# Kernel optimization log

Hardware: AMD Instinct MI355X
Metric: run time of the kernel (lower is better)

## Reference

```python
import jax, jax.numpy as jnp
import numpy as np

K = 256
HEADS = 4

def setup_inputs() -> dict:
    key = jax.random.key(0)
    ks = jax.random.split(key, 6)
    x = jax.random.normal(ks[0], (4, 4096, K), dtype=jnp.float32)
    scale = 1.0 / np.sqrt(K)
    Wq = jax.random.normal(ks[1], (K, K), dtype=jnp.float32) * scale
    Wk = jax.random.normal(ks[2], (K, K), dtype=jnp.float32) * scale
    Wv = jax.random.normal(ks[3], (K, K), dtype=jnp.float32) * scale
    Wu = jax.random.normal(ks[4], (K, K), dtype=jnp.float32) * scale
    bu = jax.random.normal(ks[5], (K,), dtype=jnp.float32) * scale
    return {"x": x, "Wq": Wq, "Wk": Wk, "Wv": Wv, "Wu": Wu, "bu": bu}

def reference(x, Wq, Wk, Wv, Wu, bu):
    b, t, e = x.shape
    h = HEADS
    s = e // h
    # torch Linear: y = x @ W.T
    q = (x @ Wq.T).reshape(b, t, h, s)
    k = (x @ Wk.T).reshape(b, t, h, s)
    v = (x @ Wv.T).reshape(b, t, h, s)
    # scores: [b, h, t, t]
    dot = jnp.einsum('bihs,bjhs->bhij', q, k) / jnp.sqrt(jnp.float32(s))
    # NOTE: original code calls masked_fill (non in-place) and discards the
    # result, so the causal mask has NO effect. Faithful: no mask.
    attn = jax.nn.softmax(dot, axis=-1)
    out = jnp.einsum('bhij,bjhs->bihs', attn, v).reshape(b, t, e)
    return out @ Wu.T + bu
```

## Files before the change

### kernel.cpp

```cpp
#include <hip/hip_runtime.h>

typedef unsigned short u16;
typedef __attribute__((ext_vector_type(8))) __bf16 bf16x8;
typedef __attribute__((ext_vector_type(4))) float f32x4;
typedef __attribute__((ext_vector_type(4))) unsigned int u32x4;
typedef __attribute__((ext_vector_type(2))) unsigned int u32x2;

#define GLD16(g, l) __builtin_amdgcn_global_load_lds( \
    (const __attribute__((address_space(1))) unsigned int*)(g), \
    (__attribute__((address_space(3))) unsigned int*)(l), 16, 0, 0)

__device__ __forceinline__ u16 f2bf(float f) {
    unsigned u = __builtin_bit_cast(unsigned, f);
    unsigned r = u + 0x7fffu + ((u >> 16) & 1u);
    return (u16)(r >> 16);
}

__global__ __launch_bounds__(256) void cvt_bf16(const float* __restrict__ src,
                                                u16* __restrict__ dst, int n8) {
    int i = blockIdx.x * 256 + threadIdx.x;
    if (i >= n8) return;
    const float4* s = (const float4*)src;
    float4 a = s[2 * i], b = s[2 * i + 1];
    union { u16 u[8]; u32x4 v; } o;
    o.u[0] = f2bf(a.x); o.u[1] = f2bf(a.y); o.u[2] = f2bf(a.z); o.u[3] = f2bf(a.w);
    o.u[4] = f2bf(b.x); o.u[5] = f2bf(b.y); o.u[6] = f2bf(b.z); o.u[7] = f2bf(b.w);
    ((u32x4*)dst)[i] = o.v;
}

__global__ __launch_bounds__(256) void cvt_w4(const float* __restrict__ Wq,
                                              const float* __restrict__ Wk,
                                              const float* __restrict__ Wv,
                                              const float* __restrict__ Wu,
                                              u16* __restrict__ dst, float qscale) {
    int i = blockIdx.x * 256 + threadIdx.x;
    int widx = i >> 13, j = i & 8191;
    const float* src = (widx == 0) ? Wq : (widx == 1) ? Wk : (widx == 2) ? Wv : Wu;
    float scale = (widx == 0) ? qscale : 1.0f;
    const float4* s = (const float4*)src;
    float4 a = s[2 * j], b = s[2 * j + 1];
    union { u16 u[8]; u32x4 v; } o;
    o.u[0] = f2bf(a.x * scale); o.u[1] = f2bf(a.y * scale);
    o.u[2] = f2bf(a.z * scale); o.u[3] = f2bf(a.w * scale);
    o.u[4] = f2bf(b.x * scale); o.u[5] = f2bf(b.y * scale);
    o.u[6] = f2bf(b.z * scale); o.u[7] = f2bf(b.w * scale);
    ((u32x4*)dst)[i] = o.v;
}

template <int F32OUT>
__device__ __forceinline__ void gemm_core(const u16* __restrict__ A,
                                          const u16* __restrict__ B,
                                          void* __restrict__ Cout,
                                          const float* __restrict__ bias,
                                          size_t ldc, u16* As, u16* Bs) {
    const int tid = threadIdx.x;
    const int w = tid >> 6, l = tid & 63;
    const int lo = l & 15, hi = l >> 4;
    const size_t m0 = (size_t)blockIdx.x * 128;
    const int n0 = blockIdx.y * 128;
    const int wm = (w >> 1) * 64, wn = (w & 1) * 64;

    f32x4 acc[4][4] = {};

    {
#pragma unroll
        for (int i = 0; i < 2; ++i) {
            int cidx = (w * 2 + i) * 64 + l;
            int row = cidx >> 2, c = cidx & 3;
            GLD16(A + (m0 + row) * 256 + c * 8, &As[(w * 2 + i) * 512]);
            GLD16(B + (size_t)(n0 + row) * 256 + c * 8, &Bs[(w * 2 + i) * 512]);
        }
    }
    int buf = 0;
#pragma unroll 1
    for (int k0 = 0; k0 < 8; ++k0) {
        __syncthreads();
        if (k0 < 7) {
#pragma unroll
            for (int i = 0; i < 2; ++i) {
                int cidx = (w * 2 + i) * 64 + l;
                int row = cidx >> 2, c = cidx & 3;
                GLD16(A + (m0 + row) * 256 + (k0 + 1) * 32 + c * 8, &As[(buf ^ 1) * 4096 + (w * 2 + i) * 512]);
                GLD16(B + (size_t)(n0 + row) * 256 + (k0 + 1) * 32 + c * 8, &Bs[(buf ^ 1) * 4096 + (w * 2 + i) * 512]);
            }
        }
        bf16x8 af[4], bg[4];
#pragma unroll
        for (int mt = 0; mt < 4; ++mt)
            af[mt] = *(const bf16x8*)&As[buf * 4096 + (wm + mt * 16 + lo) * 32 + hi * 8];
#pragma unroll
        for (int nt = 0; nt < 4; ++nt)
            bg[nt] = *(const bf16x8*)&Bs[buf * 4096 + (wn + nt * 16 + lo) * 32 + hi * 8];
        __builtin_amdgcn_s_setprio(1);
#pragma unroll
        for (int mt = 0; mt < 4; ++mt)
#pragma unroll
            for (int nt = 0; nt < 4; ++nt)
                acc[mt][nt] = __builtin_amdgcn_mfma_f32_16x16x32_bf16(af[mt], bg[nt], acc[mt][nt], 0, 0, 0);
        __builtin_amdgcn_s_setprio(0);
        buf ^= 1;
    }

    const int r0 = hi * 4;
#pragma unroll
    for (int mt = 0; mt < 4; ++mt) {
#pragma unroll
        for (int nt = 0; nt < 4; ++nt) {
            int col = n0 + wn + nt * 16 + lo;
#pragma unroll
            for (int r = 0; r < 4; ++r) {
                size_t row = m0 + wm + mt * 16 + r0 + r;
                if (F32OUT) {
                    ((float*)Cout)[row * ldc + col] = acc[mt][nt][r] + bias[col];
                } else {
                    ((u16*)Cout)[row * ldc + col] = f2bf(acc[mt][nt][r]);
                }
            }
        }
    }
}

__global__ __launch_bounds__(256) void gemm_qk(const u16* __restrict__ xb,
                                               const u16* __restrict__ wqb,
                                               const u16* __restrict__ wkb,
                                               u16* __restrict__ qb,
                                               u16* __restrict__ kb) {
    __shared__ u16 As[2 * 4096];
    __shared__ u16 Bs[2 * 4096];
    if (blockIdx.z == 0)
        gemm_core<0>(xb, wqb, qb, nullptr, 256, As, Bs);
    else
        gemm_core<0>(xb, wkb, kb, nullptr, 256, As, Bs);
}

template <int F32OUT>
__global__ __launch_bounds__(256) void gemm_one(const u16* __restrict__ A,
                                                const u16* __restrict__ B,
                                                void* __restrict__ C,
                                                const float* __restrict__ bias,
                                                size_t ldc) {
    __shared__ u16 As[2 * 4096];
    __shared__ u16 Bs[2 * 4096];
    gemm_core<F32OUT>(A, B, C, bias, ldc, As, Bs);
}

__global__ __launch_bounds__(256, 2) void attn_fwd(const u16* __restrict__ qb,
                                                   const u16* __restrict__ kb,
                                                   const u16* __restrict__ vtb,
                                                   u16* __restrict__ attb) {
    __shared__ u16 Ks[2][64 * 64];
    __shared__ u16 Vs[2][64 * 64];
    __shared__ u16 Ps[4][32 * 64];
    const int tid = threadIdx.x, w = tid >> 6, l = tid & 63;
    const int lo = l & 15, hi = l >> 4;

    int lin = blockIdx.y * gridDim.x + blockIdx.x;
    int nid = (lin & 7) * 64 + (lin >> 3);
    const int bh = nid >> 5, qblk = nid & 31;
    const int b = bh >> 2, h = bh & 3;
    const int qbase = qblk * 128 + w * 32;

    bf16x8 qf[2][2];
#pragma unroll
    for (int mt = 0; mt < 2; ++mt)
#pragma unroll
        for (int ks = 0; ks < 2; ++ks)
            qf[mt][ks] = *(const bf16x8*)&qb[(size_t)(b * 4096 + qbase + mt * 16 + lo) * 256 + h * 64 + ks * 32 + hi * 8];

    float lsum[2] = {0.f, 0.f};
    f32x4 o[2][4] = {};
    const f32x4 fz = {0.f, 0.f, 0.f, 0.f};

    auto stage = [&](int sb, int kt) {
#pragma unroll
        for (int i = 0; i < 2; ++i) {
            int cidx = (w * 2 + i) * 64 + l;
            int row = cidx >> 3, c = cidx & 7;
            int sc = c ^ (row & 7);
            GLD16(kb + (size_t)(b * 4096 + kt * 64 + row) * 256 + h * 64 + sc * 8,
                  &Ks[sb][(w * 2 + i) * 512]);
            GLD16(vtb + (size_t)(h * 64 + row) * 16384 + (size_t)b * 4096 + kt * 64 + sc * 8,
                  &Vs[sb][(w * 2 + i) * 512]);
        }
    };

    stage(0, 0);
    int buf = 0;
#pragma unroll 1
    for (int kt = 0; kt < 64; ++kt) {
        __syncthreads();
        if (kt < 63) stage(buf ^ 1, kt + 1);

        f32x4 s[2][4];
        {
            bf16x8 kf[4];
#pragma unroll
            for (int nt = 0; nt < 4; ++nt) {
                int key = nt * 16 + lo;
                int pc = hi ^ (key & 7);
                kf[nt] = *(const bf16x8*)&Ks[buf][key * 64 + pc * 8];
            }
            __builtin_amdgcn_s_setprio(1);
#pragma unroll
            for (int mt = 0; mt < 2; ++mt)
#pragma unroll
                for (int nt = 0; nt < 4; ++nt)
                    s[mt][nt] = __builtin_amdgcn_mfma_f32_16x16x32_bf16(kf[nt], qf[mt][0], fz, 0, 0, 0);
            __builtin_amdgcn_s_setprio(0);
        }
        {
            bf16x8 kf[4];
#pragma unroll
            for (int nt = 0; nt < 4; ++nt) {
                int key = nt * 16 + lo;
                int pc = (4 + hi) ^ (key & 7);
                kf[nt] = *(const bf16x8*)&Ks[buf][key * 64 + pc * 8];
            }
            __builtin_amdgcn_s_setprio(1);
#pragma unroll
            for (int mt = 0; mt < 2; ++mt)
#pragma unroll
                for (int nt = 0; nt < 4; ++nt)
                    s[mt][nt] = __builtin_amdgcn_mfma_f32_16x16x32_bf16(kf[nt], qf[mt][1], s[mt][nt], 0, 0, 0);
            __builtin_amdgcn_s_setprio(0);
        }

#pragma unroll
        for (int mt = 0; mt < 2; ++mt) {
#pragma unroll
            for (int nt = 0; nt < 4; ++nt) {
                union { __bf16 bb[4]; u32x2 v; } pw;
#pragma unroll
                for (int r = 0; r < 4; ++r) {
                    float p = __builtin_amdgcn_exp2f(s[mt][nt][r]);
                    lsum[mt] += p;
                    pw.bb[r] = (__bf16)p;
                }
                *(u32x2*)&Ps[w][(mt * 16 + lo) * 64 + (((nt * 4 + hi) ^ lo) << 2)] = pw.v;
            }
        }
        asm volatile("s_waitcnt lgkmcnt(0)" ::: "memory");

#pragma unroll
        for (int ks2 = 0; ks2 < 2; ++ks2) {
            bf16x8 vf[4];
#pragma unroll
            for (int dt = 0; dt < 4; ++dt) {
                int dr = dt * 16 + lo;
                vf[dt] = *(const bf16x8*)&Vs[buf][dr * 64 + (((ks2 * 4 + hi) ^ (dr & 7)) << 3)];
            }
            union { u32x2 c[2]; bf16x8 v; } pA, pB;
            pA.c[0] = *(const u32x2*)&Ps[w][(0 + lo) * 64 + (((ks2 * 8 + hi * 2 + 0) ^ lo) << 2)];
            pA.c[1] = *(const u32x2*)&Ps[w][(0 + lo) * 64 + (((ks2 * 8 + hi * 2 + 1) ^ lo) << 2)];
            pB.c[0] = *(const u32x2*)&Ps[w][(16 + lo) * 64 + (((ks2 * 8 + hi * 2 + 0) ^ lo) << 2)];
            pB.c[1] = *(const u32x2*)&Ps[w][(16 + lo) * 64 + (((ks2 * 8 + hi * 2 + 1) ^ lo) << 2)];
            __builtin_amdgcn_s_setprio(1);
#pragma unroll
            for (int dt = 0; dt < 4; ++dt)
                o[0][dt] = __builtin_amdgcn_mfma_f32_16x16x32_bf16(vf[dt], pA.v, o[0][dt], 0, 0, 0);
#pragma unroll
            for (int dt = 0; dt < 4; ++dt)
                o[1][dt] = __builtin_amdgcn_mfma_f32_16x16x32_bf16(vf[dt], pB.v, o[1][dt], 0, 0, 0);
            __builtin_amdgcn_s_setprio(0);
        }
        buf ^= 1;
    }

#pragma unroll
    for (int mt = 0; mt < 2; ++mt) {
        float ls = lsum[mt];
        ls += __shfl_xor(ls, 16);
        ls += __shfl_xor(ls, 32);
        float inv = __builtin_amdgcn_rcpf(ls);
        size_t row = (size_t)(b * 4096 + qbase + mt * 16 + lo);
#pragma unroll
        for (int dt = 0; dt < 4; ++dt) {
            union { __bf16 bb[4]; u32x2 v; } ob;
#pragma unroll
            for (int r = 0; r < 4; ++r) ob.bb[r] = (__bf16)(o[mt][dt][r] * inv);
            *(u32x2*)&attb[row * 256 + h * 64 + dt * 16 + hi * 4] = ob.v;
        }
    }
}

extern "C" void kernel_launch(void* const* d_in, const int* in_sizes, int n_in,
                              void* d_out, int out_size, void* d_ws, size_t ws_size,
                              hipStream_t stream) {
    const float* x  = (const float*)d_in[0];
    const float* Wq = (const float*)d_in[1];
    const float* Wk = (const float*)d_in[2];
    const float* Wv = (const float*)d_in[3];
    const float* Wu = (const float*)d_in[4];
    const float* bu = (const float*)d_in[5];

    char* ws = (char*)d_ws;
    u16* xb  = (u16*)ws;
    u16* qb  = (u16*)(ws + (8u << 20));
    u16* kb  = (u16*)(ws + (16u << 20));
    u16* vtb = (u16*)(ws + (24u << 20));
    u16* wqb = (u16*)(ws + (32u << 20));
    u16* wkb = wqb + 65536;
    u16* wvb = wkb + 65536;
    u16* wub = wvb + 65536;
    u16* attb = xb;

    const float kLog2eOver8 = 0.18033688011112042f;

    cvt_bf16<<<2048, 256, 0, stream>>>(x, xb, in_sizes[0] / 8);
    cvt_w4<<<128, 256, 0, stream>>>(Wq, Wk, Wv, Wu, wqb, kLog2eOver8);

    gemm_qk<<<dim3(128, 2, 2), 256, 0, stream>>>(xb, wqb, wkb, qb, kb);
    gemm_one<0><<<dim3(2, 128), 256, 0, stream>>>(wvb, xb, vtb, nullptr, 16384);

    attn_fwd<<<dim3(32, 16), 256, 0, stream>>>(qb, kb, vtb, attb);

    gemm_one<1><<<dim3(128, 2), 256, 0, stream>>>(attb, wub, d_out, bu, 256);
}
```

Measured before the change: 133.2 us.

## Triple-buffer attention K/V staging, compute row sums via MFMA, fuse QKV GEMMs

The attention kernel moves from double to triple buffering of K/V tiles. It waits with vmcnt and a raw barrier instead of a full __syncthreads, so loads run two tiles ahead. The softmax denominator is now computed by an extra MFMA against a vector of ones instead of scalar adds plus cross-lane shuffles. The V projection GEMM is folded into the Q/K launch as a third grid slice, which removes one kernel launch. Costs are more LDS per block, which may reduce occupancy at 2 blocks/CU, and bf16 rounding of P now also enters the row sum.

```diff
diff --git a/kernel.cpp b/kernel.cpp
--- a/kernel.cpp
+++ b/kernel.cpp
@@ -52,12 +52,13 @@
                                           const u16* __restrict__ B,
                                           void* __restrict__ Cout,
                                           const float* __restrict__ bias,
-                                          size_t ldc, u16* As, u16* Bs) {
+                                          size_t ldc, int mblk, int nblk,
+                                          u16* As, u16* Bs) {
     const int tid = threadIdx.x;
     const int w = tid >> 6, l = tid & 63;
     const int lo = l & 15, hi = l >> 4;
-    const size_t m0 = (size_t)blockIdx.x * 128;
-    const int n0 = blockIdx.y * 128;
+    const size_t m0 = (size_t)mblk * 128;
+    const int n0 = nblk * 128;
     const int wm = (w >> 1) * 64, wn = (w & 1) * 64;
 
     f32x4 acc[4][4] = {};
@@ -120,17 +121,21 @@
     }
 }
 
-__global__ __launch_bounds__(256) void gemm_qk(const u16* __restrict__ xb,
-                                               const u16* __restrict__ wqb,
-                                               const u16* __restrict__ wkb,
-                                               u16* __restrict__ qb,
-                                               u16* __restrict__ kb) {
+__global__ __launch_bounds__(256) void gemm_qkv(const u16* __restrict__ xb,
+                                                const u16* __restrict__ wqb,
+                                                const u16* __restrict__ wkb,
+                                                const u16* __restrict__ wvb,
+                                                u16* __restrict__ qb,
+                                                u16* __restrict__ kb,
+                                                u16* __restrict__ vtb) {
     __shared__ u16 As[2 * 4096];
     __shared__ u16 Bs[2 * 4096];
     if (blockIdx.z == 0)
-        gemm_core<0>(xb, wqb, qb, nullptr, 256, As, Bs);
+        gemm_core<0>(xb, wqb, qb, nullptr, 256, blockIdx.x, blockIdx.y, As, Bs);
+    else if (blockIdx.z == 1)
+        gemm_core<0>(xb, wkb, kb, nullptr, 256, blockIdx.x, blockIdx.y, As, Bs);
     else
-        gemm_core<0>(xb, wkb, kb, nullptr, 256, As, Bs);
+        gemm_core<0>(wvb, xb, vtb, nullptr, 16384, blockIdx.y, blockIdx.x, As, Bs);
 }
 
 template <int F32OUT>
@@ -141,15 +146,15 @@
                                                 size_t ldc) {
     __shared__ u16 As[2 * 4096];
     __shared__ u16 Bs[2 * 4096];
-    gemm_core<F32OUT>(A, B, C, bias, ldc, As, Bs);
+    gemm_core<F32OUT>(A, B, C, bias, ldc, blockIdx.x, blockIdx.y, As, Bs);
 }
 
 __global__ __launch_bounds__(256, 2) void attn_fwd(const u16* __restrict__ qb,
                                                    const u16* __restrict__ kb,
                                                    const u16* __restrict__ vtb,
                                                    u16* __restrict__ attb) {
-    __shared__ u16 Ks[2][64 * 64];
-    __shared__ u16 Vs[2][64 * 64];
+    __shared__ u16 Ks[3][64 * 64];
+    __shared__ u16 Vs[3][64 * 64];
     __shared__ u16 Ps[4][32 * 64];
     const int tid = threadIdx.x, w = tid >> 6, l = tid & 63;
     const int lo = l & 15, hi = l >> 4;
@@ -167,8 +172,12 @@
         for (int ks = 0; ks < 2; ++ks)
             qf[mt][ks] = *(const bf16x8*)&qb[(size_t)(b * 4096 + qbase + mt * 16 + lo) * 256 + h * 64 + ks * 32 + hi * 8];
 
-    float lsum[2] = {0.f, 0.f};
+    bf16x8 ones;
+#pragma unroll
+    for (int j = 0; j < 8; ++j) ones[j] = (__bf16)1.0f;
+
     f32x4 o[2][4] = {};
+    f32x4 osum[2] = {};
     const f32x4 fz = {0.f, 0.f, 0.f, 0.f};
 
     auto stage = [&](int sb, int kt) {
@@ -185,11 +194,14 @@
     };
 
     stage(0, 0);
-    int buf = 0;
+    stage(1, 1);
 #pragma unroll 1
     for (int kt = 0; kt < 64; ++kt) {
-        __syncthreads();
-        if (kt < 63) stage(buf ^ 1, kt + 1);
+        if (kt < 63) { asm volatile("s_waitcnt vmcnt(4)" ::: "memory"); }
+        else         { asm volatile("s_waitcnt vmcnt(0)" ::: "memory"); }
+        __builtin_amdgcn_s_barrier();
+        if (kt < 62) stage((kt + 2) % 3, kt + 2);
+        const int sl = kt % 3;
 
         f32x4 s[2][4];
         {
@@ -198,7 +210,7 @@
             for (int nt = 0; nt < 4; ++nt) {
                 int key = nt * 16 + lo;
                 int pc = hi ^ (key & 7);
-                kf[nt] = *(const bf16x8*)&Ks[buf][key * 64 + pc * 8];
+                kf[nt] = *(const bf16x8*)&Ks[sl][key * 64 + pc * 8];
             }
             __builtin_amdgcn_s_setprio(1);
 #pragma unroll
@@ -214,7 +226,7 @@
             for (int nt = 0; nt < 4; ++nt) {
                 int key = nt * 16 + lo;
                 int pc = (4 + hi) ^ (key & 7);
-                kf[nt] = *(const bf16x8*)&Ks[buf][key * 64 + pc * 8];
+                kf[nt] = *(const bf16x8*)&Ks[sl][key * 64 + pc * 8];
             }
             __builtin_amdgcn_s_setprio(1);
 #pragma unroll
@@ -231,11 +243,8 @@
             for (int nt = 0; nt < 4; ++nt) {
                 union { __bf16 bb[4]; u32x2 v; } pw;
 #pragma unroll
-                for (int r = 0; r < 4; ++r) {
-                    float p = __builtin_amdgcn_exp2f(s[mt][nt][r]);
-                    lsum[mt] += p;
-                    pw.bb[r] = (__bf16)p;
-                }
+                for (int r = 0; r < 4; ++r)
+                    pw.bb[r] = (__bf16)__builtin_amdgcn_exp2f(s[mt][nt][r]);
                 *(u32x2*)&Ps[w][(mt * 16 + lo) * 64 + (((nt * 4 + hi) ^ lo) << 2)] = pw.v;
             }
         }
@@ -247,7 +256,7 @@
 #pragma unroll
             for (int dt = 0; dt < 4; ++dt) {
                 int dr = dt * 16 + lo;
-                vf[dt] = *(const bf16x8*)&Vs[buf][dr * 64 + (((ks2 * 4 + hi) ^ (dr & 7)) << 3)];
+                vf[dt] = *(const bf16x8*)&Vs[sl][dr * 64 + (((ks2 * 4 + hi) ^ (dr & 7)) << 3)];
             }
             union { u32x2 c[2]; bf16x8 v; } pA, pB;
             pA.c[0] = *(const u32x2*)&Ps[w][(0 + lo) * 64 + (((ks2 * 8 + hi * 2 + 0) ^ lo) << 2)];
@@ -261,17 +270,15 @@
 #pragma unroll
             for (int dt = 0; dt < 4; ++dt)
                 o[1][dt] = __builtin_amdgcn_mfma_f32_16x16x32_bf16(vf[dt], pB.v, o[1][dt], 0, 0, 0);
+            osum[0] = __builtin_amdgcn_mfma_f32_16x16x32_bf16(ones, pA.v, osum[0], 0, 0, 0);
+            osum[1] = __builtin_amdgcn_mfma_f32_16x16x32_bf16(ones, pB.v, osum[1], 0, 0, 0);
             __builtin_amdgcn_s_setprio(0);
         }
-        buf ^= 1;
     }
 
 #pragma unroll
     for (int mt = 0; mt < 2; ++mt) {
-        float ls = lsum[mt];
-        ls += __shfl_xor(ls, 16);
-        ls += __shfl_xor(ls, 32);
-        float inv = __builtin_amdgcn_rcpf(ls);
+        float inv = __builtin_amdgcn_rcpf(osum[mt][0]);
         size_t row = (size_t)(b * 4096 + qbase + mt * 16 + lo);
 #pragma unroll
         for (int dt = 0; dt < 4; ++dt) {
@@ -309,8 +316,7 @@
     cvt_bf16<<<2048, 256, 0, stream>>>(x, xb, in_sizes[0] / 8);
     cvt_w4<<<128, 256, 0, stream>>>(Wq, Wk, Wv, Wu, wqb, kLog2eOver8);
 
-    gemm_qk<<<dim3(128, 2, 2), 256, 0, stream>>>(xb, wqb, wkb, qb, kb);
-    gemm_one<0><<<dim3(2, 128), 256, 0, stream>>>(wvb, xb, vtb, nullptr, 16384);
+    gemm_qkv<<<dim3(128, 2, 3), 256, 0, stream>>>(xb, wqb, wkb, wvb, qb, kb, vtb);
 
     attn_fwd<<<dim3(32, 16), 256, 0, stream>>>(qb, kb, vtb, attb);
 
```

Result: faster. 126.2 us (-5.3%).

## Split attention over key halves, fuse QKV GEMMs, merge partials in output GEMM

Applied to the files above, without the earlier changes.

The attention kernel gains a split over the key dimension (grid z), so 1024 workgroups each process half the keys. Each writes normalized partial outputs in a per-head layout plus row sums. A small kernel turns the row sums into merge weights, and a new output GEMM blends the two partials while loading its A tile. The Q, K and V projections are merged into one launch, occupancy hints for attention go up, and the P reload is restructured per m-tile. This adds workspace traffic, an extra launch and register-staged A loads in exchange for better CU fill in attention.

```diff
diff --git a/kernel.cpp b/kernel.cpp
--- a/kernel.cpp
+++ b/kernel.cpp
@@ -52,12 +52,13 @@
                                           const u16* __restrict__ B,
                                           void* __restrict__ Cout,
                                           const float* __restrict__ bias,
-                                          size_t ldc, u16* As, u16* Bs) {
+                                          size_t ldc, int mblk, int nblk,
+                                          u16* As, u16* Bs) {
     const int tid = threadIdx.x;
     const int w = tid >> 6, l = tid & 63;
     const int lo = l & 15, hi = l >> 4;
-    const size_t m0 = (size_t)blockIdx.x * 128;
-    const int n0 = blockIdx.y * 128;
+    const size_t m0 = (size_t)mblk * 128;
+    const int n0 = nblk * 128;
     const int wm = (w >> 1) * 64, wn = (w & 1) * 64;
 
     f32x4 acc[4][4] = {};
@@ -120,37 +121,140 @@
     }
 }
 
-__global__ __launch_bounds__(256) void gemm_qk(const u16* __restrict__ xb,
-                                               const u16* __restrict__ wqb,
-                                               const u16* __restrict__ wkb,
-                                               u16* __restrict__ qb,
-                                               u16* __restrict__ kb) {
+__global__ __launch_bounds__(256) void gemm_qkv(const u16* __restrict__ xb,
+                                                const u16* __restrict__ wqb,
+                                                const u16* __restrict__ wkb,
+                                                const u16* __restrict__ wvb,
+                                                u16* __restrict__ qb,
+                                                u16* __restrict__ kb,
+                                                u16* __restrict__ vtb) {
     __shared__ u16 As[2 * 4096];
     __shared__ u16 Bs[2 * 4096];
     if (blockIdx.z == 0)
-        gemm_core<0>(xb, wqb, qb, nullptr, 256, As, Bs);
+        gemm_core<0>(xb, wqb, qb, nullptr, 256, blockIdx.x, blockIdx.y, As, Bs);
+    else if (blockIdx.z == 1)
+        gemm_core<0>(xb, wkb, kb, nullptr, 256, blockIdx.x, blockIdx.y, As, Bs);
     else
-        gemm_core<0>(xb, wkb, kb, nullptr, 256, As, Bs);
-}
-
-template <int F32OUT>
-__global__ __launch_bounds__(256) void gemm_one(const u16* __restrict__ A,
-                                                const u16* __restrict__ B,
-                                                void* __restrict__ C,
-                                                const float* __restrict__ bias,
-                                                size_t ldc) {
-    __shared__ u16 As[2 * 4096];
-    __shared__ u16 Bs[2 * 4096];
-    gemm_core<F32OUT>(A, B, C, bias, ldc, As, Bs);
-}
-
-__global__ __launch_bounds__(256, 2) void attn_fwd(const u16* __restrict__ qb,
+        gemm_core<0>(wvb, xb, vtb, nullptr, 16384, blockIdx.y, blockIdx.x, As, Bs);
+}
+
+__global__ __launch_bounds__(256) void wcombine(const float* __restrict__ L,
+                                                float2* __restrict__ wbuf) {
+    int i = blockIdx.x * 256 + threadIdx.x;
+    float l0 = L[i], l1 = L[65536 + i];
+    float inv = __builtin_amdgcn_rcpf(l0 + l1);
+    wbuf[i] = make_float2(l0 * inv, l1 * inv);
+}
+
+template <int NS>
+__global__ __launch_bounds__(256) void gemm_out(const u16* __restrict__ O0,
+                                                const u16* __restrict__ O1,
+                                                const float2* __restrict__ wbuf,
+                                                const u16* __restrict__ Wu,
+                                                float* __restrict__ out,
+                                                const float* __restrict__ bias) {
+    __shared__ u16 As[2][4096];
+    __shared__ u16 Bs[2][4096];
+    const int tid = threadIdx.x, w = tid >> 6, l = tid & 63;
+    const int lo = l & 15, hi = l >> 4;
+    const size_t m0 = (size_t)blockIdx.x * 128;
+    const int n0 = blockIdx.y * 128;
+    const int wm = (w >> 1) * 64, wn = (w & 1) * 64;
+    f32x4 acc[4][4] = {};
+
+    u32x4 aA[2], aB[2];
+    float2 awt[2];
+    auto loadA = [&](int k0) {
+#pragma unroll
+        for (int it = 0; it < 2; ++it) {
+            int s = it * 256 + tid;
+            int row = s >> 2, f8 = s & 3;
+            size_t grow = m0 + row;
+            int b = (int)(grow >> 12), q = (int)(grow & 4095);
+            int feat = k0 * 32 + f8 * 8;
+            int bh = b * 4 + (feat >> 6);
+            size_t oidx = ((size_t)bh * 4096 + q) * 64 + (feat & 63);
+            aA[it] = *(const u32x4*)(O0 + oidx);
+            if (NS == 2) {
+                aB[it] = *(const u32x4*)(O1 + oidx);
+                awt[it] = wbuf[(size_t)bh * 4096 + q];
+            }
+        }
+    };
+    auto writeA = [&](int buf) {
+#pragma unroll
+        for (int it = 0; it < 2; ++it) {
+            int s = it * 256 + tid;
+            int row = s >> 2, f8 = s & 3;
+            u32x4 v;
+            if (NS == 2) {
+                union { u32x4 v; __bf16 b[8]; } x, y, z;
+                x.v = aA[it]; y.v = aB[it];
+#pragma unroll
+                for (int j = 0; j < 8; ++j)
+                    z.b[j] = (__bf16)(awt[it].x * (float)x.b[j] + awt[it].y * (float)y.b[j]);
+                v = z.v;
+            } else {
+                v = aA[it];
+            }
+            *(u32x4*)&As[buf][row * 32 + f8 * 8] = v;
+        }
+    };
+    auto stageB = [&](int k0, int buf) {
+#pragma unroll
+        for (int i = 0; i < 2; ++i) {
+            int cidx = (w * 2 + i) * 64 + l;
+            int row = cidx >> 2, c = cidx & 3;
+            GLD16(Wu + (size_t)(n0 + row) * 256 + k0 * 32 + c * 8, &Bs[buf][(w * 2 + i) * 512]);
+        }
+    };
+
+    loadA(0); stageB(0, 0); writeA(0);
+#pragma unroll 1
+    for (int k0 = 0; k0 < 8; ++k0) {
+        int cur = k0 & 1, nb = cur ^ 1;
+        __syncthreads();
+        if (k0 < 7) { stageB(k0 + 1, nb); loadA(k0 + 1); }
+        bf16x8 af[4], bg[4];
+#pragma unroll
+        for (int mt = 0; mt < 4; ++mt)
+            af[mt] = *(const bf16x8*)&As[cur][(wm + mt * 16 + lo) * 32 + hi * 8];
+#pragma unroll
+        for (int nt = 0; nt < 4; ++nt)
+            bg[nt] = *(const bf16x8*)&Bs[cur][(wn + nt * 16 + lo) * 32 + hi * 8];
+        __builtin_amdgcn_s_setprio(1);
+#pragma unroll
+        for (int mt = 0; mt < 4; ++mt)
+#pragma unroll
+            for (int nt = 0; nt < 4; ++nt)
+                acc[mt][nt] = __builtin_amdgcn_mfma_f32_16x16x32_bf16(af[mt], bg[nt], acc[mt][nt], 0, 0, 0);
+        __builtin_amdgcn_s_setprio(0);
+        if (k0 < 7) writeA(nb);
+    }
+
+    const int r0 = hi * 4;
+#pragma unroll
+    for (int mt = 0; mt < 4; ++mt)
+#pragma unroll
+        for (int nt = 0; nt < 4; ++nt) {
+            int col = n0 + wn + nt * 16 + lo;
+#pragma unroll
+            for (int r = 0; r < 4; ++r) {
+                size_t row = m0 + wm + mt * 16 + r0 + r;
+                out[row * 256 + col] = acc[mt][nt][r] + bias[col];
+            }
+        }
+}
+
+__global__ __launch_bounds__(256, 4) void attn_fwd(const u16* __restrict__ qb,
                                                    const u16* __restrict__ kb,
                                                    const u16* __restrict__ vtb,
-                                                   u16* __restrict__ attb) {
-    __shared__ u16 Ks[2][64 * 64];
-    __shared__ u16 Vs[2][64 * 64];
-    __shared__ u16 Ps[4][32 * 64];
+                                                   u16* __restrict__ opart,
+                                                   float* __restrict__ lpart,
+                                                   int NT) {
+    __shared__ u16 Ks[2 * 4096];
+    __shared__ u16 Vs[2 * 4096];
+    __shared__ u16 Ps[4 * 1024];
     const int tid = threadIdx.x, w = tid >> 6, l = tid & 63;
     const int lo = l & 15, hi = l >> 4;
 
@@ -159,6 +263,9 @@
     const int bh = nid >> 5, qblk = nid & 31;
     const int b = bh >> 2, h = bh & 3;
     const int qbase = qblk * 128 + w * 32;
+    const int kt0 = blockIdx.z * NT;
+    u16* Oh = opart + (size_t)blockIdx.z * 4194304;
+    float* Lh = lpart + blockIdx.z * 65536;
 
     bf16x8 qf[2][2];
 #pragma unroll
@@ -178,18 +285,18 @@
             int row = cidx >> 3, c = cidx & 7;
             int sc = c ^ (row & 7);
             GLD16(kb + (size_t)(b * 4096 + kt * 64 + row) * 256 + h * 64 + sc * 8,
-                  &Ks[sb][(w * 2 + i) * 512]);
+                  &Ks[sb * 4096 + (w * 2 + i) * 512]);
             GLD16(vtb + (size_t)(h * 64 + row) * 16384 + (size_t)b * 4096 + kt * 64 + sc * 8,
-                  &Vs[sb][(w * 2 + i) * 512]);
+                  &Vs[sb * 4096 + (w * 2 + i) * 512]);
         }
     };
 
-    stage(0, 0);
-    int buf = 0;
+    stage(0, kt0);
+    int cur = 0;
 #pragma unroll 1
-    for (int kt = 0; kt < 64; ++kt) {
+    for (int kt = 0; kt < NT; ++kt) {
         __syncthreads();
-        if (kt < 63) stage(buf ^ 1, kt + 1);
+        if (kt + 1 < NT) stage(cur ^ 1, kt0 + kt + 1);
 
         f32x4 s[2][4];
         {
@@ -197,8 +304,7 @@
 #pragma unroll
             for (int nt = 0; nt < 4; ++nt) {
                 int key = nt * 16 + lo;
-                int pc = hi ^ (key & 7);
-                kf[nt] = *(const bf16x8*)&Ks[buf][key * 64 + pc * 8];
+                kf[nt] = *(const bf16x8*)&Ks[cur * 4096 + key * 64 + (hi ^ (key & 7)) * 8];
             }
             __builtin_amdgcn_s_setprio(1);
 #pragma unroll
@@ -213,8 +319,7 @@
 #pragma unroll
             for (int nt = 0; nt < 4; ++nt) {
                 int key = nt * 16 + lo;
-                int pc = (4 + hi) ^ (key & 7);
-                kf[nt] = *(const bf16x8*)&Ks[buf][key * 64 + pc * 8];
+                kf[nt] = *(const bf16x8*)&Ks[cur * 4096 + key * 64 + ((4 + hi) ^ (key & 7)) * 8];
             }
             __builtin_amdgcn_s_setprio(1);
 #pragma unroll
@@ -225,6 +330,7 @@
             __builtin_amdgcn_s_setprio(0);
         }
 
+        bf16x8 pf[2][2];
 #pragma unroll
         for (int mt = 0; mt < 2; ++mt) {
 #pragma unroll
@@ -236,10 +342,18 @@
                     lsum[mt] += p;
                     pw.bb[r] = (__bf16)p;
                 }
-                *(u32x2*)&Ps[w][(mt * 16 + lo) * 64 + (((nt * 4 + hi) ^ lo) << 2)] = pw.v;
-            }
-        }
-        asm volatile("s_waitcnt lgkmcnt(0)" ::: "memory");
+                *(u32x2*)&Ps[w * 1024 + lo * 64 + (((nt * 4 + hi) ^ lo) << 2)] = pw.v;
+            }
+            asm volatile("s_waitcnt lgkmcnt(0)" ::: "memory");
+#pragma unroll
+            for (int ks2 = 0; ks2 < 2; ++ks2) {
+                union { u32x2 c[2]; bf16x8 v; } pu;
+                pu.c[0] = *(const u32x2*)&Ps[w * 1024 + lo * 64 + (((ks2 * 8 + hi * 2 + 0) ^ lo) << 2)];
+                pu.c[1] = *(const u32x2*)&Ps[w * 1024 + lo * 64 + (((ks2 * 8 + hi * 2 + 1) ^ lo) << 2)];
+                pf[mt][ks2] = pu.v;
+            }
+            asm volatile("s_waitcnt lgkmcnt(0)" ::: "memory");
+        }
 
 #pragma unroll
         for (int ks2 = 0; ks2 < 2; ++ks2) {
@@ -247,23 +361,18 @@
 #pragma unroll
             for (int dt = 0; dt < 4; ++dt) {
                 int dr = dt * 16 + lo;
-                vf[dt] = *(const bf16x8*)&Vs[buf][dr * 64 + (((ks2 * 4 + hi) ^ (dr & 7)) << 3)];
-            }
-            union { u32x2 c[2]; bf16x8 v; } pA, pB;
-            pA.c[0] = *(const u32x2*)&Ps[w][(0 + lo) * 64 + (((ks2 * 8 + hi * 2 + 0) ^ lo) << 2)];
-            pA.c[1] = *(const u32x2*)&Ps[w][(0 + lo) * 64 + (((ks2 * 8 + hi * 2 + 1) ^ lo) << 2)];
-            pB.c[0] = *(const u32x2*)&Ps[w][(16 + lo) * 64 + (((ks2 * 8 + hi * 2 + 0) ^ lo) << 2)];
-            pB.c[1] = *(const u32x2*)&Ps[w][(16 + lo) * 64 + (((ks2 * 8 + hi * 2 + 1) ^ lo) << 2)];
+                vf[dt] = *(const bf16x8*)&Vs[cur * 4096 + dr * 64 + (((ks2 * 4 + hi) ^ (dr & 7)) << 3)];
+            }
             __builtin_amdgcn_s_setprio(1);
 #pragma unroll
             for (int dt = 0; dt < 4; ++dt)
-                o[0][dt] = __builtin_amdgcn_mfma_f32_16x16x32_bf16(vf[dt], pA.v, o[0][dt], 0, 0, 0);
+                o[0][dt] = __builtin_amdgcn_mfma_f32_16x16x32_bf16(vf[dt], pf[0][ks2], o[0][dt], 0, 0, 0);
 #pragma unroll
             for (int dt = 0; dt < 4; ++dt)
-                o[1][dt] = __builtin_amdgcn_mfma_f32_16x16x32_bf16(vf[dt], pB.v, o[1][dt], 0, 0, 0);
+                o[1][dt] = __builtin_amdgcn_mfma_f32_16x16x32_bf16(vf[dt], pf[1][ks2], o[1][dt], 0, 0, 0);
             __builtin_amdgcn_s_setprio(0);
         }
-        buf ^= 1;
+        cur ^= 1;
     }
 
 #pragma unroll
@@ -272,14 +381,16 @@
         ls += __shfl_xor(ls, 16);
         ls += __shfl_xor(ls, 32);
         float inv = __builtin_amdgcn_rcpf(ls);
-        size_t row = (size_t)(b * 4096 + qbase + mt * 16 + lo);
+        int qrow = qbase + mt * 16 + lo;
+        size_t obase = ((size_t)bh * 4096 + qrow) * 64;
 #pragma unroll
         for (int dt = 0; dt < 4; ++dt) {
             union { __bf16 bb[4]; u32x2 v; } ob;
 #pragma unroll
             for (int r = 0; r < 4; ++r) ob.bb[r] = (__bf16)(o[mt][dt][r] * inv);
-            *(u32x2*)&attb[row * 256 + h * 64 + dt * 16 + hi * 4] = ob.v;
-        }
+            *(u32x2*)&Oh[obase + dt * 16 + hi * 4] = ob.v;
+        }
+        if (hi == 0) Lh[bh * 4096 + qrow] = ls;
     }
 }
 
@@ -302,17 +413,36 @@
     u16* wkb = wqb + 65536;
     u16* wvb = wkb + 65536;
     u16* wub = wvb + 65536;
-    u16* attb = xb;
+
+    const int nsplit = (ws_size >= (size_t)(50u << 20)) ? 2 : 1;
+    const int NT = 64 / nsplit;
+    u16* opart;
+    float* lpart;
+    float2* wbuf = nullptr;
+    if (nsplit == 2) {
+        lpart = (float*)(ws + (33u << 20));
+        wbuf  = (float2*)(ws + (33u << 20) + (512u << 10));
+        opart = (u16*)(ws + (34u << 20));
+    } else {
+        opart = xb;
+        lpart = (float*)wqb;
+    }
 
     const float kLog2eOver8 = 0.18033688011112042f;
 
     cvt_bf16<<<2048, 256, 0, stream>>>(x, xb, in_sizes[0] / 8);
     cvt_w4<<<128, 256, 0, stream>>>(Wq, Wk, Wv, Wu, wqb, kLog2eOver8);
 
-    gemm_qk<<<dim3(128, 2, 2), 256, 0, stream>>>(xb, wqb, wkb, qb, kb);
-    gemm_one<0><<<dim3(2, 128), 256, 0, stream>>>(wvb, xb, vtb, nullptr, 16384);
-
-    attn_fwd<<<dim3(32, 16), 256, 0, stream>>>(qb, kb, vtb, attb);
-
-    gemm_one<1><<<dim3(128, 2), 256, 0, stream>>>(attb, wub, d_out, bu, 256);
-}
+    gemm_qkv<<<dim3(128, 2, 3), 256, 0, stream>>>(xb, wqb, wkb, wvb, qb, kb, vtb);
+
+    attn_fwd<<<dim3(32, 16, nsplit), 256, 0, stream>>>(qb, kb, vtb, opart, lpart, NT);
+
+    if (nsplit == 2) {
+        wcombine<<<256, 256, 0, stream>>>(lpart, wbuf);
+        gemm_out<2><<<dim3(128, 2), 256, 0, stream>>>(opart, opart + 4194304, wbuf, wub,
+                                                      (float*)d_out, bu);
+    } else {
+        gemm_out<1><<<dim3(128, 2), 256, 0, stream>>>(opart, nullptr, nullptr, wub,
+                                                      (float*)d_out, bu);
+    }
+}
```

Measured after the change: 122.1 us. 1.09x faster.
